# Optimization experiments

Measured on AMD Instinct MI355X. Metric: run time of the kernel, lower is better.

Reference implementation:

```python
import jax, jax.numpy as jnp
import numpy as np
from jax import lax

TOP_K = 4
N_GROUP = 4
TOPK_GROUP = 2
ROUTED_SCALING = 2.5
NORM_TOPK = True


def relu2(v):
    r = jax.nn.relu(v)
    return r * r


def setup_inputs() -> dict:
    key = jax.random.key(0)
    ks = jax.random.split(key, 7)
    B, S, H, E, I, IS = 2, 2048, 1024, 16, 512, 2048
    x = jax.random.normal(ks[0], (B, S, H), dtype=jnp.float32)
    router_w = jax.random.normal(ks[1], (E, H), dtype=jnp.float32) * 0.02
    bias = jnp.zeros((E,), dtype=jnp.float32)
    w_up = jax.random.normal(ks[2], (E, I, H), dtype=jnp.float32) * 0.02
    w_down = jax.random.normal(ks[3], (E, H, I), dtype=jnp.float32) * 0.02
    ws_up = jax.random.normal(ks[4], (IS, H), dtype=jnp.float32) * 0.02
    ws_down = jax.random.normal(ks[5], (H, IS), dtype=jnp.float32) * 0.02
    return {"x": x, "router_w": router_w, "bias": bias, "w_up": w_up,
            "w_down": w_down, "ws_up": ws_up, "ws_down": ws_down,
            "attn_metadata": 0}


def _route(xf, router_w, bias):
    # xf: [T, H] float32
    T = xf.shape[0]
    E = router_w.shape[0]
    logits = xf @ router_w.T                      # [T, E]
    scores = jax.nn.sigmoid(logits)
    sfc = scores + bias[None, :]                  # scores_for_choice
    # group scores: sum of top-2 within each group
    g = sfc.reshape(T, N_GROUP, E // N_GROUP)
    group_scores = lax.top_k(g, 2)[0].sum(-1)     # [T, G]
    _, gidx = lax.top_k(group_scores, TOPK_GROUP)
    gmask = jax.nn.one_hot(gidx, N_GROUP, dtype=sfc.dtype).sum(1)  # [T, G]
    smask = jnp.repeat(gmask, E // N_GROUP, axis=1)                # [T, E]
    masked = jnp.where(smask > 0, sfc, 0.0)
    _, tidx = lax.top_k(masked, TOP_K)            # [T, K]
    tw = jnp.take_along_axis(scores, tidx, axis=1)
    if NORM_TOPK:
        tw = tw / (tw.sum(-1, keepdims=True) + 1e-20)
    tw = tw * ROUTED_SCALING
    return tidx, tw


def reference(x, router_w, bias, w_up, w_down, ws_up, ws_down, attn_metadata):
    B, S, H = x.shape
    E = w_up.shape[0]
    xf = x.reshape(-1, H).astype(jnp.float32)     # [T, H]
    tidx, tw = _route(xf, router_w, bias)
    # combine weights per (token, expert): scatter-add topk weights
    T = xf.shape[0]
    comb = jnp.zeros((T, E), dtype=tw.dtype).at[jnp.arange(T)[:, None], tidx].add(tw)
    # routed experts (dense grouped form; zero combine weight == not routed)
    up = jnp.einsum('th,eih->tei', xf, w_up)      # [T, E, I]
    h = relu2(up) * comb[:, :, None]
    routed = jnp.einsum('tei,ehi->th', h, w_down) # [T, H]
    routed = routed.reshape(B, S, H).astype(x.dtype)
    # shared expert on residual
    shared = relu2(jnp.einsum('bsh,ih->bsi', x, ws_up))
    shared = jnp.einsum('bsi,hi->bsh', shared, ws_down)
    return routed + shared
```

## Files before the change

kernel.cpp:

```cpp
#include <hip/hip_runtime.h>
#include <stdint.h>

#define T_TOK 4096
#define H_DIM 1024
#define E_NUM 16
#define I_DIM 512
#define IS_DIM 2048
#define TOPK 4
#define NGRP 4
#define GSZ 4
#define MAXMT 32
#define NCHUNK 64

typedef unsigned short u16;
typedef __attribute__((ext_vector_type(8))) short short8;
typedef __attribute__((ext_vector_type(4))) float f32x4;

__device__ __forceinline__ void gload16(const void* g, void* l) {
  __builtin_amdgcn_global_load_lds(
      (const __attribute__((address_space(1))) void*)g,
      (__attribute__((address_space(3))) void*)l, 16, 0, 0);
}

__device__ __forceinline__ u16 f2bf(float f) {
  union { float f; uint32_t u; } v; v.f = f;
  uint32_t u = v.u;
  uint32_t r = (u + 0x7fffu + ((u >> 16) & 1u)) >> 16;
  return (u16)r;
}

__device__ __forceinline__ float bf2f(u16 h) {
  union { uint32_t u; float f; } v; v.u = ((uint32_t)h) << 16;
  return v.f;
}

__global__ __launch_bounds__(256) void cvt_bf16_kernel(const float* __restrict__ in,
                                                       u16* __restrict__ out, int n4) {
  int i = blockIdx.x * 256 + threadIdx.x;
  if (i >= n4) return;
  float4 v = reinterpret_cast<const float4*>(in)[i];
  ushort4 o;
  o.x = f2bf(v.x); o.y = f2bf(v.y); o.z = f2bf(v.z); o.w = f2bf(v.w);
  reinterpret_cast<ushort4*>(out)[i] = o;
}

__global__ __launch_bounds__(256) void route_kernel(
    const float* __restrict__ x, const float* __restrict__ rw,
    const float* __restrict__ bias, int* __restrict__ tidx_out,
    float* __restrict__ tw_out) {
  const int wave = threadIdx.x >> 6;
  const int lane = threadIdx.x & 63;
  const int t = blockIdx.x * 4 + wave;

  const float4* xr = reinterpret_cast<const float4*>(x + (size_t)t * H_DIM);
  const float4* rw4 = reinterpret_cast<const float4*>(rw);
  float4 xv[4];
#pragma unroll
  for (int j = 0; j < 4; ++j) xv[j] = xr[lane + j * 64];

  double acc[E_NUM];
#pragma unroll
  for (int e = 0; e < E_NUM; ++e) {
    double a = 0.0;
#pragma unroll
    for (int j = 0; j < 4; ++j) {
      float4 w = rw4[e * 256 + lane + j * 64];
      a += (double)xv[j].x * (double)w.x;
      a += (double)xv[j].y * (double)w.y;
      a += (double)xv[j].z * (double)w.z;
      a += (double)xv[j].w * (double)w.w;
    }
    acc[e] = a;
  }
#pragma unroll
  for (int e = 0; e < E_NUM; ++e) {
#pragma unroll
    for (int off = 32; off; off >>= 1) acc[e] += __shfl_xor(acc[e], off);
  }
  if (lane == 0) {
    float scores[E_NUM], sfc[E_NUM];
#pragma unroll
    for (int e = 0; e < E_NUM; ++e) {
      scores[e] = 1.0f / (1.0f + expf((float)(-acc[e])));
      sfc[e] = scores[e] + bias[e];
    }
    float gs[NGRP];
#pragma unroll
    for (int g = 0; g < NGRP; ++g) {
      float m1 = -1e30f, m2 = -1e30f;
#pragma unroll
      for (int j = 0; j < GSZ; ++j) {
        float v = sfc[g * GSZ + j];
        if (v > m1) { m2 = m1; m1 = v; } else if (v > m2) { m2 = v; }
      }
      gs[g] = m1 + m2;
    }
    int g1 = 0;
    for (int g = 1; g < NGRP; ++g) if (gs[g] > gs[g1]) g1 = g;
    int g2 = -1;
    for (int g = 0; g < NGRP; ++g) {
      if (g == g1) continue;
      if (g2 < 0 || gs[g] > gs[g2]) g2 = g;
    }
    float masked[E_NUM];
#pragma unroll
    for (int e = 0; e < E_NUM; ++e) {
      int g = e / GSZ;
      masked[e] = (g == g1 || g == g2) ? sfc[e] : 0.0f;
    }
    int tidx[TOPK]; float tw[TOPK];
#pragma unroll
    for (int k = 0; k < TOPK; ++k) {
      int best = 0; float bv = masked[0];
      for (int e = 1; e < E_NUM; ++e)
        if (masked[e] > bv) { bv = masked[e]; best = e; }
      tidx[k] = best; tw[k] = scores[best]; masked[best] = -1e30f;
    }
    float s = tw[0] + tw[1] + tw[2] + tw[3] + 1e-20f;
#pragma unroll
    for (int k = 0; k < TOPK; ++k) {
      tidx_out[t * TOPK + k] = tidx[k];
      tw_out[t * TOPK + k] = tw[k] / s * 2.5f;
    }
  }
}

__global__ __launch_bounds__(256) void hist_kernel(const int* __restrict__ tidx,
                                                   int* __restrict__ partial) {
  const int c = blockIdx.x;
  const int tid = threadIdx.x;
  const int lane = tid & 63;
  const int w = tid >> 6;
  __shared__ int h[4][E_NUM];
  const int e = tidx[c * 256 + tid];
#pragma unroll
  for (int ee = 0; ee < E_NUM; ++ee) {
    unsigned long long b = __ballot(e == ee);
    if (lane == 0) h[w][ee] = __popcll(b);
  }
  __syncthreads();
  if (tid < E_NUM)
    partial[c * E_NUM + tid] = h[0][tid] + h[1][tid] + h[2][tid] + h[3][tid];
}

__global__ __launch_bounds__(256) void prefix2_kernel(
    const int* __restrict__ partial, int* __restrict__ chunk_base,
    int* __restrict__ counts, int* __restrict__ offsets) {
  __shared__ int tot[E_NUM];
  __shared__ int offs[E_NUM];
  const int tid = threadIdx.x;
  if (tid < E_NUM) {
    int run = 0;
    for (int c = 0; c < NCHUNK; ++c) {
      chunk_base[c * E_NUM + tid] = run;
      run += partial[c * E_NUM + tid];
    }
    tot[tid] = run;
    counts[tid] = run;
  }
  __syncthreads();
  if (tid == 0) {
    int s = 0;
    for (int e = 0; e < E_NUM; ++e) { offs[e] = s; offsets[e] = s; s += tot[e]; }
    offsets[E_NUM] = s;
  }
  __syncthreads();
  for (int i = tid; i < NCHUNK * E_NUM; i += 256)
    chunk_base[i] += offs[i & 15];
}

__global__ __launch_bounds__(256) void scatter2_kernel(
    const int* __restrict__ tidx, const float* __restrict__ tw,
    const int* __restrict__ chunk_base,
    int* __restrict__ tok_g, float* __restrict__ w_g, int* __restrict__ pos_map) {
  const int c = blockIdx.x;
  const int tid = threadIdx.x;
  const int lane = tid & 63;
  const int w = tid >> 6;
  __shared__ int h[4][E_NUM];
  const int i = c * 256 + tid;
  const int e = tidx[i];
  int pre = 0;
#pragma unroll
  for (int ee = 0; ee < E_NUM; ++ee) {
    unsigned long long b = __ballot(e == ee);
    if (lane == 0) h[w][ee] = __popcll(b);
    if (ee == e) pre = __popcll(b & ((1ull << lane) - 1ull));
  }
  __syncthreads();
  int rank = pre;
  for (int ww = 0; ww < w; ++ww) rank += h[ww][e];
  const int pos = chunk_base[c * E_NUM + e] + rank;
  tok_g[pos] = i >> 2;
  w_g[pos] = tw[i];
  pos_map[i] = pos;
}

template <int EPI>
__global__ __launch_bounds__(512, 4) void gemm_bt(
    const u16* __restrict__ Abase, const u16* __restrict__ Bbase,
    float* __restrict__ Cf, u16* __restrict__ Cb,
    int M, int N, int K,
    const int* __restrict__ counts, const int* __restrict__ offsets,
    const int* __restrict__ tok_g, const float* __restrict__ w_g,
    const int* __restrict__ pos_map, const u16* __restrict__ Rd) {
  __shared__ __align__(16) u16 As[2][128 * 64];
  __shared__ __align__(16) u16 Bs[2][128 * 64];

  const int NT = N >> 7;
  int mt, nt, cnt = M, obase = 0;
  const u16* A = Abase;
  const u16* B = Bbase;

  if constexpr (EPI <= 1) {
    mt = blockIdx.x / NT;
    nt = blockIdx.x - mt * NT;
  } else {
    const int per_e = MAXMT * NT;
    int e = blockIdx.x / per_e;
    int r = blockIdx.x - e * per_e;
    mt = r / NT;
    nt = r - mt * NT;
    cnt = counts[e];
    if (mt * 128 >= cnt) return;
    obase = offsets[e];
    if constexpr (EPI == 2) {
      B = Bbase + (size_t)e * (I_DIM * H_DIM);
    } else {
      A = Abase + (size_t)obase * I_DIM;
      B = Bbase + (size_t)e * (H_DIM * I_DIM);
    }
  }

  const int tid = threadIdx.x;
  const int srow = tid >> 3;
  const int slot = tid & 7;
  const u16* gA[2];
  const u16* gB[2];
#pragma unroll
  for (int p = 0; p < 2; ++p) {
    int rloc = p * 64 + srow;
    int ks = ((slot ^ (rloc & 7)) << 3);
    int am = mt * 128 + rloc;
    if constexpr (EPI == 2) {
      int tk = tok_g[obase + ((am < cnt) ? am : 0)];
      gA[p] = Abase + (size_t)tk * H_DIM + ks;
    } else if constexpr (EPI == 3) {
      gA[p] = A + (size_t)((am < cnt) ? am : 0) * K + ks;
    } else {
      gA[p] = A + (size_t)am * K + ks;
    }
    gB[p] = B + (size_t)(nt * 128 + rloc) * K + ks;
  }

  const int wave = tid >> 6;
  const int lane = tid & 63;
  const int wr = wave >> 2;
  const int wc = wave & 3;
  const int frow = lane & 15;
  const int l4 = lane >> 4;

  int a_off[4][2], b_off[2][2];
#pragma unroll
  for (int m = 0; m < 4; ++m) {
    int row = wr * 64 + m * 16 + frow;
#pragma unroll
    for (int kk = 0; kk < 2; ++kk)
      a_off[m][kk] = (row << 6) + ((((kk << 2) + l4) ^ (row & 7)) << 3);
  }
#pragma unroll
  for (int n = 0; n < 2; ++n) {
    int row = wc * 32 + n * 16 + frow;
#pragma unroll
    for (int kk = 0; kk < 2; ++kk)
      b_off[n][kk] = (row << 6) + ((((kk << 2) + l4) ^ (row & 7)) << 3);
  }

  f32x4 acc[4][2];
#pragma unroll
  for (int m = 0; m < 4; ++m)
#pragma unroll
    for (int n = 0; n < 2; ++n) acc[m][n] = (f32x4)0.0f;

  const int dst = tid << 3;
  auto stage = [&](int k0, int c) {
#pragma unroll
    for (int p = 0; p < 2; ++p)
      gload16(gA[p] + k0, &As[c][(p << 12) + dst]);
#pragma unroll
    for (int p = 0; p < 2; ++p)
      gload16(gB[p] + k0, &Bs[c][(p << 12) + dst]);
  };

  const int KT = K >> 6;
  stage(0, 0);
  int cur = 0;
  for (int kt = 0; kt < KT; ++kt) {
    __syncthreads();
    if (kt + 1 < KT) stage((kt + 1) << 6, cur ^ 1);
#pragma unroll
    for (int kk = 0; kk < 2; ++kk) {
      short8 a[4], b[2];
#pragma unroll
      for (int m = 0; m < 4; ++m)
        a[m] = *reinterpret_cast<const short8*>(&As[cur][a_off[m][kk]]);
#pragma unroll
      for (int n = 0; n < 2; ++n)
        b[n] = *reinterpret_cast<const short8*>(&Bs[cur][b_off[n][kk]]);
#pragma unroll
      for (int m = 0; m < 4; ++m)
#pragma unroll
        for (int n = 0; n < 2; ++n)
          acc[m][n] = __builtin_amdgcn_mfma_f32_16x16x32_bf16(a[m], b[n], acc[m][n], 0, 0, 0);
    }
    cur ^= 1;
  }

  const int rbase = l4 << 2;
  const int cbase = frow;
#pragma unroll
  for (int m = 0; m < 4; ++m) {
#pragma unroll
    for (int r = 0; r < 4; ++r) {
      int lr = wr * 64 + (m << 4) + rbase + r;
      int grow = mt * 128 + lr;
      if (EPI >= 2 && grow >= cnt) continue;
      float wv = 1.0f;
      if constexpr (EPI == 2) wv = w_g[obase + grow];
      const int* pm = nullptr;
      if constexpr (EPI == 1) pm = pos_map + grow * TOPK;
#pragma unroll
      for (int n = 0; n < 2; ++n) {
        int gc = nt * 128 + wc * 32 + (n << 4) + cbase;
        float v = acc[m][n][r];
        if constexpr (EPI == 0) {
          float tpos = fmaxf(v, 0.0f);
          Cb[(size_t)grow * N + gc] = f2bf(tpos * tpos);
        } else if constexpr (EPI == 1) {
          v += bf2f(Rd[(size_t)pm[0] * H_DIM + gc]);
          v += bf2f(Rd[(size_t)pm[1] * H_DIM + gc]);
          v += bf2f(Rd[(size_t)pm[2] * H_DIM + gc]);
          v += bf2f(Rd[(size_t)pm[3] * H_DIM + gc]);
          Cf[(size_t)grow * N + gc] = v;
        } else if constexpr (EPI == 2) {
          float tpos = fmaxf(v, 0.0f);
          Cb[(size_t)(obase + grow) * I_DIM + gc] = f2bf(tpos * tpos * wv);
        } else {
          Cb[(size_t)(obase + grow) * N + gc] = f2bf(v);
        }
      }
    }
  }
}

extern "C" void kernel_launch(void* const* d_in, const int* in_sizes, int n_in,
                              void* d_out, int out_size, void* d_ws, size_t ws_size,
                              hipStream_t stream) {
  const float* x = (const float*)d_in[0];
  const float* rw = (const float*)d_in[1];
  const float* bias = (const float*)d_in[2];
  const float* w_up = (const float*)d_in[3];
  const float* w_down = (const float*)d_in[4];
  const float* ws_up = (const float*)d_in[5];
  const float* ws_down = (const float*)d_in[6];
  float* out = (float*)d_out;

  uint8_t* wsb = (uint8_t*)d_ws;
  size_t off = 0;
  auto alloc = [&](size_t bytes) {
    void* p = wsb + off;
    off += (bytes + 255) & ~(size_t)255;
    return p;
  };
  u16* x_bf = (u16*)alloc((size_t)T_TOK * H_DIM * 2);
  u16* wsup_bf = (u16*)alloc((size_t)IS_DIM * H_DIM * 2);
  u16* wsdn_bf = (u16*)alloc((size_t)H_DIM * IS_DIM * 2);
  u16* wup_bf = (u16*)alloc((size_t)E_NUM * I_DIM * H_DIM * 2);
  u16* wdn_bf = (u16*)alloc((size_t)E_NUM * H_DIM * I_DIM * 2);
  u16* hs = (u16*)alloc((size_t)T_TOK * IS_DIM * 2);
  u16* hp = (u16*)alloc((size_t)(T_TOK * TOPK + 128) * I_DIM * 2);
  u16* hp_down = (u16*)alloc((size_t)(T_TOK * TOPK + 128) * H_DIM * 2);
  int* counts = (int*)alloc(64);
  int* offsets = (int*)alloc(128);
  int* tok_g = (int*)alloc((size_t)(T_TOK * TOPK) * 4);
  float* w_g = (float*)alloc((size_t)(T_TOK * TOPK) * 4);
  int* pos_map = (int*)alloc((size_t)(T_TOK * TOPK) * 4);
  int* tidx_buf = (int*)alloc((size_t)T_TOK * TOPK * 4);
  float* tw_buf = (float*)alloc((size_t)T_TOK * TOPK * 4);
  int* partial = (int*)alloc((size_t)NCHUNK * E_NUM * 4);
  int* chunk_base = (int*)alloc((size_t)NCHUNK * E_NUM * 4);

  int n4;
  n4 = T_TOK * H_DIM / 4;
  cvt_bf16_kernel<<<(n4 + 255) / 256, 256, 0, stream>>>(x, x_bf, n4);
  n4 = IS_DIM * H_DIM / 4;
  cvt_bf16_kernel<<<(n4 + 255) / 256, 256, 0, stream>>>(ws_up, wsup_bf, n4);
  n4 = H_DIM * IS_DIM / 4;
  cvt_bf16_kernel<<<(n4 + 255) / 256, 256, 0, stream>>>(ws_down, wsdn_bf, n4);
  n4 = E_NUM * I_DIM * H_DIM / 4;
  cvt_bf16_kernel<<<(n4 + 255) / 256, 256, 0, stream>>>(w_up, wup_bf, n4);
  n4 = E_NUM * H_DIM * I_DIM / 4;
  cvt_bf16_kernel<<<(n4 + 255) / 256, 256, 0, stream>>>(w_down, wdn_bf, n4);

  route_kernel<<<T_TOK / 4, 256, 0, stream>>>(x, rw, bias, tidx_buf, tw_buf);
  hist_kernel<<<NCHUNK, 256, 0, stream>>>(tidx_buf, partial);
  prefix2_kernel<<<1, 256, 0, stream>>>(partial, chunk_base, counts, offsets);
  scatter2_kernel<<<NCHUNK, 256, 0, stream>>>(tidx_buf, tw_buf, chunk_base,
                                              tok_g, w_g, pos_map);

  gemm_bt<0><<<(T_TOK / 128) * (IS_DIM / 128), 512, 0, stream>>>(
      x_bf, wsup_bf, nullptr, hs, T_TOK, IS_DIM, H_DIM,
      nullptr, nullptr, nullptr, nullptr, nullptr, nullptr);
  gemm_bt<2><<<E_NUM * MAXMT * (I_DIM / 128), 512, 0, stream>>>(
      x_bf, wup_bf, nullptr, hp, T_TOK, I_DIM, H_DIM,
      counts, offsets, tok_g, w_g, nullptr, nullptr);
  gemm_bt<3><<<E_NUM * MAXMT * (H_DIM / 128), 512, 0, stream>>>(
      hp, wdn_bf, nullptr, hp_down, T_TOK, H_DIM, I_DIM,
      counts, offsets, tok_g, w_g, nullptr, nullptr);
  gemm_bt<1><<<(T_TOK / 128) * (H_DIM / 128), 512, 0, stream>>>(
      hs, wsdn_bf, out, nullptr, T_TOK, H_DIM, IS_DIM,
      nullptr, nullptr, nullptr, nullptr, pos_map, hp_down);
}
```

Measured before the change: 208.1 us.

## Triple-buffer GEMM LDS pipeline, swizzle block order, and fuse bf16 conversions

The bf16 GEMM moves from double to triple buffering. It waits on vmcnt so loads run two k-steps ahead, uses a raw s_barrier, and raises wave priority around the MFMA block. Workgroup indices are remapped in interleaved order, which is meant to improve L2 locality across the eight dies, and launch bounds drop to 2 blocks per CU for the larger LDS footprint. The five separate fp32-to-bf16 conversion launches become one fused kernel to cut launch overhead. The risks are lower occupancy and an interleave that assumes the grid size is divisible by 8.

New measurement: 236.7 us. 1.14x slower.

```diff
diff --git a/kernel.cpp b/kernel.cpp
--- a/kernel.cpp
+++ b/kernel.cpp
@@ -12,6 +12,12 @@
 #define MAXMT 32
 #define NCHUNK 64
 
+#define S0 1048576
+#define S1 1572864
+#define S2 2097152
+#define S3 4194304
+#define S4 6291456
+
 typedef unsigned short u16;
 typedef __attribute__((ext_vector_type(8))) short short8;
 typedef __attribute__((ext_vector_type(4))) float f32x4;
@@ -34,14 +40,23 @@
   return v.f;
 }
 
-__global__ __launch_bounds__(256) void cvt_bf16_kernel(const float* __restrict__ in,
-                                                       u16* __restrict__ out, int n4) {
+__global__ __launch_bounds__(256) void cvt_all_kernel(
+    const float* __restrict__ x, const float* __restrict__ wsu,
+    const float* __restrict__ wsd, const float* __restrict__ wu,
+    const float* __restrict__ wd,
+    u16* __restrict__ xb, u16* __restrict__ wsub, u16* __restrict__ wsdb,
+    u16* __restrict__ wub, u16* __restrict__ wdb) {
   int i = blockIdx.x * 256 + threadIdx.x;
-  if (i >= n4) return;
-  float4 v = reinterpret_cast<const float4*>(in)[i];
+  const float4* src; ushort4* dst; int base;
+  if (i < S0)      { src = (const float4*)x;   dst = (ushort4*)xb;   base = 0;  }
+  else if (i < S1) { src = (const float4*)wsu; dst = (ushort4*)wsub; base = S0; }
+  else if (i < S2) { src = (const float4*)wsd; dst = (ushort4*)wsdb; base = S1; }
+  else if (i < S3) { src = (const float4*)wu;  dst = (ushort4*)wub;  base = S2; }
+  else             { src = (const float4*)wd;  dst = (ushort4*)wdb;  base = S3; }
+  float4 v = src[i - base];
   ushort4 o;
   o.x = f2bf(v.x); o.y = f2bf(v.y); o.z = f2bf(v.z); o.w = f2bf(v.w);
-  reinterpret_cast<ushort4*>(out)[i] = o;
+  dst[i - base] = o;
 }
 
 __global__ __launch_bounds__(256) void route_kernel(
@@ -197,15 +212,18 @@
 }
 
 template <int EPI>
-__global__ __launch_bounds__(512, 4) void gemm_bt(
+__global__ __launch_bounds__(512, 2) void gemm_bt(
     const u16* __restrict__ Abase, const u16* __restrict__ Bbase,
     float* __restrict__ Cf, u16* __restrict__ Cb,
     int M, int N, int K,
     const int* __restrict__ counts, const int* __restrict__ offsets,
     const int* __restrict__ tok_g, const float* __restrict__ w_g,
     const int* __restrict__ pos_map, const u16* __restrict__ Rd) {
-  __shared__ __align__(16) u16 As[2][128 * 64];
-  __shared__ __align__(16) u16 Bs[2][128 * 64];
+  __shared__ __align__(16) u16 As[3][128 * 64];
+  __shared__ __align__(16) u16 Bs[3][128 * 64];
+
+  const int cpx = gridDim.x >> 3;
+  const int wg = (blockIdx.x & 7) * cpx + (blockIdx.x >> 3);
 
   const int NT = N >> 7;
   int mt, nt, cnt = M, obase = 0;
@@ -213,12 +231,12 @@
   const u16* B = Bbase;
 
   if constexpr (EPI <= 1) {
-    mt = blockIdx.x / NT;
-    nt = blockIdx.x - mt * NT;
+    mt = wg / NT;
+    nt = wg - mt * NT;
   } else {
     const int per_e = MAXMT * NT;
-    int e = blockIdx.x / per_e;
-    int r = blockIdx.x - e * per_e;
+    int e = wg / per_e;
+    int r = wg - e * per_e;
     mt = r / NT;
     nt = r - mt * NT;
     cnt = counts[e];
@@ -294,26 +312,38 @@
 
   const int KT = K >> 6;
   stage(0, 0);
-  int cur = 0;
+  stage(64, 1);
+  int cb = 0, sb = 2;
   for (int kt = 0; kt < KT; ++kt) {
-    __syncthreads();
-    if (kt + 1 < KT) stage((kt + 1) << 6, cur ^ 1);
+    if (kt < KT - 1) {
+      asm volatile("s_waitcnt vmcnt(4)" ::: "memory");
+    } else {
+      asm volatile("s_waitcnt vmcnt(0)" ::: "memory");
+    }
+    __builtin_amdgcn_s_barrier();
+    __builtin_amdgcn_sched_barrier(0);
+    if (kt + 2 < KT) stage((kt + 2) << 6, sb);
+    const u16* Ab = &As[cb][0];
+    const u16* Bb = &Bs[cb][0];
 #pragma unroll
     for (int kk = 0; kk < 2; ++kk) {
       short8 a[4], b[2];
 #pragma unroll
       for (int m = 0; m < 4; ++m)
-        a[m] = *reinterpret_cast<const short8*>(&As[cur][a_off[m][kk]]);
+        a[m] = *reinterpret_cast<const short8*>(Ab + a_off[m][kk]);
 #pragma unroll
       for (int n = 0; n < 2; ++n)
-        b[n] = *reinterpret_cast<const short8*>(&Bs[cur][b_off[n][kk]]);
+        b[n] = *reinterpret_cast<const short8*>(Bb + b_off[n][kk]);
+      __builtin_amdgcn_s_setprio(1);
 #pragma unroll
       for (int m = 0; m < 4; ++m)
 #pragma unroll
         for (int n = 0; n < 2; ++n)
           acc[m][n] = __builtin_amdgcn_mfma_f32_16x16x32_bf16(a[m], b[n], acc[m][n], 0, 0, 0);
-    }
-    cur ^= 1;
+      __builtin_amdgcn_s_setprio(0);
+    }
+    cb = (cb == 2) ? 0 : cb + 1;
+    sb = (sb == 2) ? 0 : sb + 1;
   }
 
   const int rbase = l4 << 2;
@@ -390,17 +420,9 @@
   int* partial = (int*)alloc((size_t)NCHUNK * E_NUM * 4);
   int* chunk_base = (int*)alloc((size_t)NCHUNK * E_NUM * 4);
 
-  int n4;
-  n4 = T_TOK * H_DIM / 4;
-  cvt_bf16_kernel<<<(n4 + 255) / 256, 256, 0, stream>>>(x, x_bf, n4);
-  n4 = IS_DIM * H_DIM / 4;
-  cvt_bf16_kernel<<<(n4 + 255) / 256, 256, 0, stream>>>(ws_up, wsup_bf, n4);
-  n4 = H_DIM * IS_DIM / 4;
-  cvt_bf16_kernel<<<(n4 + 255) / 256, 256, 0, stream>>>(ws_down, wsdn_bf, n4);
-  n4 = E_NUM * I_DIM * H_DIM / 4;
-  cvt_bf16_kernel<<<(n4 + 255) / 256, 256, 0, stream>>>(w_up, wup_bf, n4);
-  n4 = E_NUM * H_DIM * I_DIM / 4;
-  cvt_bf16_kernel<<<(n4 + 255) / 256, 256, 0, stream>>>(w_down, wdn_bf, n4);
+  cvt_all_kernel<<<S4 / 256, 256, 0, stream>>>(
+      x, ws_up, ws_down, w_up, w_down,
+      x_bf, wsup_bf, wsdn_bf, wup_bf, wdn_bf);
 
   route_kernel<<<T_TOK / 4, 256, 0, stream>>>(x, rw, bias, tidx_buf, tw_buf);
   hist_kernel<<<NCHUNK, 256, 0, stream>>>(tidx_buf, partial);
```
